# Kernel tuning notes

Measured on AMD Instinct MI355X. Metric: run time of the kernel, lower is better.

The kernel has to match this reference:

```python
import jax, jax.numpy as jnp
import numpy as np
import math

B, S, H = 2, 2048, 1024
NH, HD = 16, 64
MAX_SCALE = 4


def setup_inputs() -> dict:
    key = jax.random.key(0)
    ks = jax.random.split(key, 8)
    s = 0.02
    return {
        "x": jax.random.normal(ks[0], (B, S, H), dtype=jnp.float32),
        "Wqkv": jax.random.normal(ks[1], (H, 3 * H), dtype=jnp.float32) * s,
        "bqkv": jnp.zeros((3 * H,), dtype=jnp.float32),
        "Wout": jax.random.normal(ks[2], (H, H), dtype=jnp.float32) * s,
        "bout": jnp.zeros((H,), dtype=jnp.float32),
        "Wscale": jax.random.normal(ks[3], (H, MAX_SCALE), dtype=jnp.float32) * s,
        "bscale": jnp.zeros((MAX_SCALE,), dtype=jnp.float32),
    }


def reference(x, Wqkv, bqkv, Wout, bout, Wscale, bscale):
    b, s, h = x.shape
    inv_sqrt_hd = 1.0 / math.sqrt(HD)
    # qkv projection -> [3, b, nh, s, hd]
    qkv = (x @ Wqkv + bqkv).reshape(b, s, 3, NH, HD).transpose(2, 0, 3, 1, 4)
    q, k, v = qkv[0], qkv[1], qkv[2]
    # per-token soft weights over scales [b, s, max_scale]
    scale_weights = jax.nn.softmax(x @ Wscale + bscale, axis=-1)
    out = jnp.zeros((b, NH, s, HD), dtype=x.dtype)
    for scale_idx in range(MAX_SCALE):
        dilation = 2 ** scale_idx
        kd = k[:, :, ::dilation]  # strided (dilated) gather of keys
        vd = v[:, :, ::dilation]
        scores = jnp.einsum("bhqd,bhkd->bhqk", q, kd) * inv_sqrt_hd
        attn = jax.nn.softmax(scores, axis=-1)
        o = jnp.einsum("bhqk,bhkd->bhqd", attn, vd)
        w = scale_weights[:, :, scale_idx][:, None, :, None]  # [b,1,s,1]
        out = out + o * w
    out = out.transpose(0, 2, 1, 3).reshape(b, s, h)
    return out @ Wout + bout
```

## Files before the change

kernel.cpp:

```cpp
#include <hip/hip_runtime.h>
#include <stdint.h>

typedef unsigned short u16;
typedef __attribute__((ext_vector_type(8))) __bf16 bf8v;
typedef __attribute__((ext_vector_type(4))) float f4v;
typedef __attribute__((ext_vector_type(16))) float f16v;

#define BB 2
#define SS 2048
#define HH 1024

#define OFF_Q   0u
#define OFF_K0  8388608u
#define OFF_K1  16777216u
#define OFF_K2  20971520u
#define OFF_K3  23068672u
#define OFF_V0  24117248u
#define OFF_V1  32505856u
#define OFF_V2  36700160u
#define OFF_V3  38797312u
#define OFF_WQT 39845888u
#define OFF_WOT 46137344u
#define OFF_SCW 48234496u

__device__ __forceinline__ u16 f2bf(float f) {
    union { float f; uint32_t u; } v; v.f = f;
    uint32_t r = v.u + 0x7fffu + ((v.u >> 16) & 1u);
    return (u16)(r >> 16);
}
__device__ __forceinline__ uint32_t pk2(float a, float b) {
    return (uint32_t)f2bf(a) | ((uint32_t)f2bf(b) << 16);
}

__global__ __launch_bounds__(256) void wconv_kernel(const float* __restrict__ W,
                                                    u16* __restrict__ Wt,
                                                    int N, int K) {
    __shared__ float tile[64][69];
    const int tid = threadIdx.x;
    const int n0 = blockIdx.x * 64, k0 = blockIdx.y * 64;
    const int r = tid >> 4, c4 = (tid & 15) * 4;
#pragma unroll
    for (int it = 0; it < 4; it++) {
        float4 v = *(const float4*)&W[(size_t)(k0 + it * 16 + r) * N + n0 + c4];
        tile[it * 16 + r][c4 + 0] = v.x; tile[it * 16 + r][c4 + 1] = v.y;
        tile[it * 16 + r][c4 + 2] = v.z; tile[it * 16 + r][c4 + 3] = v.w;
    }
    __syncthreads();
#pragma unroll
    for (int it = 0; it < 4; it++) {
        int n = it * 16 + r;
        uint2 pk;
        pk.x = pk2(tile[c4 + 0][n], tile[c4 + 1][n]);
        pk.y = pk2(tile[c4 + 2][n], tile[c4 + 3][n]);
        *(uint2*)&Wt[(size_t)(n0 + n) * K + k0 + c4] = pk;
    }
}

__global__ __launch_bounds__(256) void scale_kernel(const float* __restrict__ x,
                                                    const float* __restrict__ Wscale,
                                                    const float* __restrict__ bscale,
                                                    float* __restrict__ scw) {
    const int lane = threadIdx.x & 63;
    const int wid  = threadIdx.x >> 6;
    const int row  = blockIdx.x * 4 + wid;
    float a0 = 0.f, a1 = 0.f, a2 = 0.f, a3 = 0.f;
    for (int i = 0; i < 16; i++) {
        int hh = lane + i * 64;
        float xs = x[(size_t)row * HH + hh];
        float4 wv = *(const float4*)&Wscale[hh * 4];
        a0 += xs * wv.x; a1 += xs * wv.y; a2 += xs * wv.z; a3 += xs * wv.w;
    }
    for (int off = 1; off < 64; off <<= 1) {
        a0 += __shfl_xor(a0, off); a1 += __shfl_xor(a1, off);
        a2 += __shfl_xor(a2, off); a3 += __shfl_xor(a3, off);
    }
    if (lane == 0) {
        a0 += bscale[0]; a1 += bscale[1]; a2 += bscale[2]; a3 += bscale[3];
        float mx = fmaxf(fmaxf(a0, a1), fmaxf(a2, a3));
        float e0 = __expf(a0 - mx), e1 = __expf(a1 - mx);
        float e2 = __expf(a2 - mx), e3 = __expf(a3 - mx);
        float inv = 1.f / (e0 + e1 + e2 + e3);
        float4 o = {e0 * inv, e1 * inv, e2 * inv, e3 * inv};
        *(float4*)&scw[(size_t)row * 4] = o;
    }
}

template<int MODE, bool ABF16>
__global__ __launch_bounds__(256) void gemm_bt(const void* __restrict__ Ap,
                                               const u16* __restrict__ Bt,
                                               const float* __restrict__ bias,
                                               void* __restrict__ Cp,
                                               int N, int K) {
    __shared__ __align__(16) u16 At[128 * 40];
    __shared__ __align__(16) u16 Btl[128 * 40];
    const int tid  = threadIdx.x;
    const int lane = tid & 63;
    const int wid  = tid >> 6;
    const int l15  = lane & 15;
    const int quad = lane >> 4;
    const int wm = wid & 1, wn = wid >> 1;
    const int m0 = blockIdx.y * 128;
    const int n0 = blockIdx.x * 128;
    const int srow = tid >> 2;
    const int sc8  = (tid & 3) * 8;

    f4v acc[4][4];
#pragma unroll
    for (int i = 0; i < 4; i++)
#pragma unroll
        for (int j = 0; j < 4; j++) acc[i][j] = (f4v){0.f, 0.f, 0.f, 0.f};

    uint4 pa0, pa1;
    float4 fa00, fa01, fa10, fa11;
    if (ABF16) {
        const u16* Ab = (const u16*)Ap;
        pa0 = *(const uint4*)(Ab + (size_t)(m0 + srow) * K + sc8);
        pa1 = *(const uint4*)(Ab + (size_t)(m0 + srow + 64) * K + sc8);
    } else {
        const float* Af = (const float*)Ap;
        fa00 = *(const float4*)(Af + (size_t)(m0 + srow) * K + sc8);
        fa01 = *(const float4*)(Af + (size_t)(m0 + srow) * K + sc8 + 4);
        fa10 = *(const float4*)(Af + (size_t)(m0 + srow + 64) * K + sc8);
        fa11 = *(const float4*)(Af + (size_t)(m0 + srow + 64) * K + sc8 + 4);
    }
    uint4 pb0 = *(const uint4*)(Bt + (size_t)(n0 + srow) * K + sc8);
    uint4 pb1 = *(const uint4*)(Bt + (size_t)(n0 + srow + 64) * K + sc8);

    for (int kc = 0; kc < K; kc += 32) {
        __syncthreads();
        if (ABF16) {
            *(uint4*)&At[srow * 40 + sc8]        = pa0;
            *(uint4*)&At[(srow + 64) * 40 + sc8] = pa1;
        } else {
            uint4 w0, w1;
            w0.x = pk2(fa00.x, fa00.y); w0.y = pk2(fa00.z, fa00.w);
            w0.z = pk2(fa01.x, fa01.y); w0.w = pk2(fa01.z, fa01.w);
            w1.x = pk2(fa10.x, fa10.y); w1.y = pk2(fa10.z, fa10.w);
            w1.z = pk2(fa11.x, fa11.y); w1.w = pk2(fa11.z, fa11.w);
            *(uint4*)&At[srow * 40 + sc8]        = w0;
            *(uint4*)&At[(srow + 64) * 40 + sc8] = w1;
        }
        *(uint4*)&Btl[srow * 40 + sc8]        = pb0;
        *(uint4*)&Btl[(srow + 64) * 40 + sc8] = pb1;
        __syncthreads();
        if (kc + 32 < K) {
            if (ABF16) {
                const u16* Ab = (const u16*)Ap;
                pa0 = *(const uint4*)(Ab + (size_t)(m0 + srow) * K + kc + 32 + sc8);
                pa1 = *(const uint4*)(Ab + (size_t)(m0 + srow + 64) * K + kc + 32 + sc8);
            } else {
                const float* Af = (const float*)Ap;
                fa00 = *(const float4*)(Af + (size_t)(m0 + srow) * K + kc + 32 + sc8);
                fa01 = *(const float4*)(Af + (size_t)(m0 + srow) * K + kc + 32 + sc8 + 4);
                fa10 = *(const float4*)(Af + (size_t)(m0 + srow + 64) * K + kc + 32 + sc8);
                fa11 = *(const float4*)(Af + (size_t)(m0 + srow + 64) * K + kc + 32 + sc8 + 4);
            }
            pb0 = *(const uint4*)(Bt + (size_t)(n0 + srow) * K + kc + 32 + sc8);
            pb1 = *(const uint4*)(Bt + (size_t)(n0 + srow + 64) * K + kc + 32 + sc8);
        }
        bf8v af[4], bf[4];
#pragma unroll
        for (int t = 0; t < 4; t++) {
            af[t] = *(const bf8v*)&At[(wm * 64 + t * 16 + l15) * 40 + quad * 8];
            bf[t] = *(const bf8v*)&Btl[(wn * 64 + t * 16 + l15) * 40 + quad * 8];
        }
#pragma unroll
        for (int ti = 0; ti < 4; ti++)
#pragma unroll
            for (int tj = 0; tj < 4; tj++)
                acc[ti][tj] = __builtin_amdgcn_mfma_f32_16x16x32_bf16(af[ti], bf[tj], acc[ti][tj], 0, 0, 0);
    }

    if (MODE == 0) {
#pragma unroll
        for (int ti = 0; ti < 4; ti++)
#pragma unroll
            for (int tj = 0; tj < 4; tj++)
#pragma unroll
                for (int r = 0; r < 4; r++) {
                    int m = m0 + wm * 64 + ti * 16 + quad * 4 + r;
                    int n = n0 + wn * 64 + tj * 16 + l15;
                    ((float*)Cp)[(size_t)m * N + n] = acc[ti][tj][r] + bias[n];
                }
    } else {
        char* ws = (char*)Cp;
        u16* Qd = (u16*)ws;
        u16* K0 = (u16*)(ws + OFF_K0); u16* K1 = (u16*)(ws + OFF_K1);
        u16* K2 = (u16*)(ws + OFF_K2); u16* K3 = (u16*)(ws + OFF_K3);
        u16* V0 = (u16*)(ws + OFF_V0); u16* V1 = (u16*)(ws + OFF_V1);
        u16* V2 = (u16*)(ws + OFF_V2); u16* V3 = (u16*)(ws + OFF_V3);
        const int region = n0 >> 10;
        if (region == 0) {
#pragma unroll
            for (int ti = 0; ti < 4; ti++)
#pragma unroll
                for (int tj = 0; tj < 4; tj++)
#pragma unroll
                    for (int r = 0; r < 4; r++) {
                        int m = m0 + wm * 64 + ti * 16 + quad * 4 + r;
                        int n = n0 + wn * 64 + tj * 16 + l15;
                        Qd[(size_t)m * 1024 + n] = f2bf(acc[ti][tj][r] + bias[n]);
                    }
        } else if (region == 1) {
#pragma unroll
            for (int ti = 0; ti < 4; ti++)
#pragma unroll
                for (int tj = 0; tj < 4; tj++) {
                    int n  = n0 + wn * 64 + tj * 16 + l15;
                    int nk = n - 1024;
                    int h = nk >> 6, hd = nk & 63;
#pragma unroll
                    for (int r = 0; r < 4; r++) {
                        int m = m0 + wm * 64 + ti * 16 + quad * 4 + r;
                        int bb = m >> 11, tok = m & 2047;
                        int bh = bb * 16 + h;
                        u16 bv = f2bf((acc[ti][tj][r] + bias[n]) * 0.125f);
                        K0[((size_t)bh * 2048 + tok) * 64 + hd] = bv;
                        if (!(r & 1)) K1[((size_t)bh * 1024 + (tok >> 1)) * 64 + hd] = bv;
                        if (r == 0) {
                            K2[((size_t)bh * 512 + (tok >> 2)) * 64 + hd] = bv;
                            if (!(quad & 1)) K3[((size_t)bh * 256 + (tok >> 3)) * 64 + hd] = bv;
                        }
                    }
                }
        } else {
#pragma unroll
            for (int ti = 0; ti < 4; ti++)
#pragma unroll
                for (int tj = 0; tj < 4; tj++) {
                    int n  = n0 + wn * 64 + tj * 16 + l15;
                    int nv = n - 2048;
                    int h = nv >> 6, hd = nv & 63;
                    int tokb = m0 + wm * 64 + ti * 16 + quad * 4;
                    int bb = tokb >> 11, tok = tokb & 2047;
                    int bh = bb * 16 + h;
                    float v0 = acc[ti][tj][0] + bias[n];
                    float v1 = acc[ti][tj][1] + bias[n];
                    float v2 = acc[ti][tj][2] + bias[n];
                    float v3 = acc[ti][tj][3] + bias[n];
                    u16 c0 = f2bf(v0), c1 = f2bf(v1), c2 = f2bf(v2), c3 = f2bf(v3);
                    uint2 pk;
                    pk.x = (uint32_t)c0 | ((uint32_t)c1 << 16);
                    pk.y = (uint32_t)c2 | ((uint32_t)c3 << 16);
                    *(uint2*)&V0[((size_t)bh * 64 + hd) * 2048 + tok] = pk;
                    *(uint32_t*)&V1[((size_t)bh * 64 + hd) * 1024 + (tok >> 1)] =
                        (uint32_t)c0 | ((uint32_t)c2 << 16);
                    V2[((size_t)bh * 64 + hd) * 512 + (tok >> 2)] = c0;
                    if (!(quad & 1)) V3[((size_t)bh * 64 + hd) * 256 + (tok >> 3)] = c0;
                }
        }
    }
}

__global__ __launch_bounds__(128, 1) void attn_kernel(const char* __restrict__ ws) {
    __shared__ __align__(16) u16 Kt[32 * 72];
    __shared__ __align__(16) u16 Vt[64 * 40];
    __shared__ __align__(16) u16 Pt[2 * 64 * 40];

    const u16* Qd    = (const u16*)(ws + OFF_Q);
    const float* scw = (const float*)(ws + OFF_SCW);
    u16* attnb       = (u16*)(ws + OFF_Q);

    const int tid  = threadIdx.x;
    const int lane = tid & 63;
    const int wid  = tid >> 6;
    const int l31  = lane & 31;
    const int half = lane >> 5;
    const int b = blockIdx.z, h = blockIdx.y;
    const int qb = blockIdx.x * 128 + wid * 64;
    const int bh = b * 16 + h;

    const int skey = tid >> 3;
    const int shd8 = (tid & 7) * 8;
    const int svhd = tid >> 2;
    const int svk8 = (tid & 3) * 8;

    bf8v qf[2][4];
#pragma unroll
    for (int qt = 0; qt < 2; qt++)
#pragma unroll
        for (int ks = 0; ks < 4; ks++)
            qf[qt][ks] = *(const bf8v*)(Qd + (size_t)(b * SS + qb + qt * 32 + l31) * 1024
                                        + h * 64 + ks * 16 + half * 8);

    u16* Pw = Pt + wid * (64 * 40);

    f16v ofin[2][2];
#pragma unroll
    for (int qt = 0; qt < 2; qt++)
#pragma unroll
        for (int ht = 0; ht < 2; ht++)
#pragma unroll
            for (int r = 0; r < 16; r++) ofin[qt][ht][r] = 0.f;

    const uint32_t koff[4] = {OFF_K0, OFF_K1, OFF_K2, OFF_K3};
    const uint32_t voff[4] = {OFF_V0, OFF_V1, OFF_V2, OFF_V3};

#pragma unroll
    for (int s = 0; s < 4; s++) {
        const int Ss = SS >> s;
        const int nch = Ss >> 5;
        const u16* Kb = (const u16*)(ws + koff[s]) + (size_t)bh * Ss * 64;
        const u16* Vb = (const u16*)(ws + voff[s]) + (size_t)bh * 64 * Ss;

        f16v oacc[2][2];
#pragma unroll
        for (int qt = 0; qt < 2; qt++)
#pragma unroll
            for (int ht = 0; ht < 2; ht++)
#pragma unroll
                for (int r = 0; r < 16; r++) oacc[qt][ht][r] = 0.f;
        float ls0 = 0.f, ls1 = 0.f;

        uint4 kr0 = *(const uint4*)(Kb + (size_t)skey * 64 + shd8);
        uint4 kr1 = *(const uint4*)(Kb + (size_t)(skey + 16) * 64 + shd8);
        uint4 vr0 = *(const uint4*)(Vb + (size_t)svhd * Ss + svk8);
        uint4 vr1 = *(const uint4*)(Vb + (size_t)(svhd + 32) * Ss + svk8);

        for (int c = 0; c < nch; c++) {
            __syncthreads();
            *(uint4*)&Kt[skey * 72 + shd8]        = kr0;
            *(uint4*)&Kt[(skey + 16) * 72 + shd8] = kr1;
            *(uint4*)&Vt[svhd * 40 + svk8]        = vr0;
            *(uint4*)&Vt[(svhd + 32) * 40 + svk8] = vr1;
            __syncthreads();
            if (c + 1 < nch) {
                kr0 = *(const uint4*)(Kb + (size_t)((c + 1) * 32 + skey) * 64 + shd8);
                kr1 = *(const uint4*)(Kb + (size_t)((c + 1) * 32 + skey + 16) * 64 + shd8);
                vr0 = *(const uint4*)(Vb + (size_t)svhd * Ss + (c + 1) * 32 + svk8);
                vr1 = *(const uint4*)(Vb + (size_t)(svhd + 32) * Ss + (c + 1) * 32 + svk8);
            }
            f16v sa0, sa1;
#pragma unroll
            for (int r = 0; r < 16; r++) { sa0[r] = 0.f; sa1[r] = 0.f; }
#pragma unroll
            for (int ks = 0; ks < 4; ks++) {
                bf8v ka = *(const bf8v*)&Kt[l31 * 72 + ks * 16 + half * 8];
                sa0 = __builtin_amdgcn_mfma_f32_32x32x16_bf16(ka, qf[0][ks], sa0, 0, 0, 0);
                sa1 = __builtin_amdgcn_mfma_f32_32x32x16_bf16(ka, qf[1][ks], sa1, 0, 0, 0);
            }
#pragma unroll
            for (int qt = 0; qt < 2; qt++) {
                const f16v& sa = qt ? sa1 : sa0;
                float e[16];
#pragma unroll
                for (int r = 0; r < 16; r++) e[r] = __expf(sa[r]);
                float acc = 0.f;
#pragma unroll
                for (int r = 0; r < 16; r++) acc += e[r];
                if (qt) ls1 += acc; else ls0 += acc;
#pragma unroll
                for (int g = 0; g < 4; g++) {
                    uint2 pk;
                    pk.x = pk2(e[g * 4 + 0], e[g * 4 + 1]);
                    pk.y = pk2(e[g * 4 + 2], e[g * 4 + 3]);
                    *(uint2*)&Pw[(qt * 32 + l31) * 40 + g * 8 + half * 4] = pk;
                }
            }
            __asm__ volatile("s_waitcnt lgkmcnt(0)" ::: "memory");
#pragma unroll
            for (int kst = 0; kst < 2; kst++) {
                bf8v pb0 = *(const bf8v*)&Pw[l31 * 40 + kst * 16 + half * 8];
                bf8v pb1 = *(const bf8v*)&Pw[(32 + l31) * 40 + kst * 16 + half * 8];
#pragma unroll
                for (int ht = 0; ht < 2; ht++) {
                    bf8v va = *(const bf8v*)&Vt[(ht * 32 + l31) * 40 + kst * 16 + half * 8];
                    oacc[0][ht] = __builtin_amdgcn_mfma_f32_32x32x16_bf16(va, pb0, oacc[0][ht], 0, 0, 0);
                    oacc[1][ht] = __builtin_amdgcn_mfma_f32_32x32x16_bf16(va, pb1, oacc[1][ht], 0, 0, 0);
                }
            }
        }
#pragma unroll
        for (int qt = 0; qt < 2; qt++) {
            float l = qt ? ls1 : ls0;
            l += __shfl_xor(l, 32);
            float w = scw[(size_t)(b * SS + qb + qt * 32 + l31) * 4 + s] / l;
#pragma unroll
            for (int ht = 0; ht < 2; ht++)
#pragma unroll
                for (int r = 0; r < 16; r++) ofin[qt][ht][r] += w * oacc[qt][ht][r];
        }
    }
#pragma unroll
    for (int qt = 0; qt < 2; qt++) {
        const size_t base = (size_t)(b * SS + qb + qt * 32 + l31) * 1024 + h * 64;
#pragma unroll
        for (int ht = 0; ht < 2; ht++)
#pragma unroll
            for (int g = 0; g < 4; g++) {
                uint2 pk;
                pk.x = pk2(ofin[qt][ht][g * 4 + 0], ofin[qt][ht][g * 4 + 1]);
                pk.y = pk2(ofin[qt][ht][g * 4 + 2], ofin[qt][ht][g * 4 + 3]);
                *(uint2*)&attnb[base + ht * 32 + g * 8 + half * 4] = pk;
            }
    }
}

extern "C" void kernel_launch(void* const* d_in, const int* in_sizes, int n_in,
                              void* d_out, int out_size, void* d_ws, size_t ws_size,
                              hipStream_t stream) {
    const float* x      = (const float*)d_in[0];
    const float* Wqkv   = (const float*)d_in[1];
    const float* bqkv   = (const float*)d_in[2];
    const float* Wout   = (const float*)d_in[3];
    const float* bout   = (const float*)d_in[4];
    const float* Wscale = (const float*)d_in[5];
    const float* bscale = (const float*)d_in[6];
    float* out = (float*)d_out;

    char* ws = (char*)d_ws;
    u16*   wqt   = (u16*)(ws + OFF_WQT);
    u16*   wot   = (u16*)(ws + OFF_WOT);
    u16*   attnb = (u16*)(ws + OFF_Q);
    float* scw   = (float*)(ws + OFF_SCW);

    wconv_kernel<<<dim3(48, 16), dim3(256), 0, stream>>>(Wqkv, wqt, 3072, 1024);
    wconv_kernel<<<dim3(16, 16), dim3(256), 0, stream>>>(Wout, wot, 1024, 1024);
    scale_kernel<<<dim3(1024), dim3(256), 0, stream>>>(x, Wscale, bscale, scw);
    gemm_bt<1, false><<<dim3(24, 32), dim3(256), 0, stream>>>(
        (const void*)x, wqt, bqkv, (void*)ws, 3072, 1024);
    attn_kernel<<<dim3(16, 16, 2), dim3(128), 0, stream>>>(ws);
    gemm_bt<0, true><<<dim3(8, 32), dim3(256), 0, stream>>>(
        (const void*)attnb, wot, bout, (void*)out, 1024, 1024);
}
```

Measured before the change: 314.2 us.

## Split attention scales across waves, per-wave LDS, pre-convert x to bf16

The attention kernel now gives each block 64 queries and splits the scales between its two waves. Wave 0 handles the full-length scale 0 and wave 1 handles the dilated scales 1 to 3, so the two waves do roughly equal work. Each wave gets its own LDS region for K, V and P, which removes the block-wide syncthreads inside the chunk loop. The two partial outputs are combined through LDS at the end, the grid is doubled, and launch bounds allow two blocks per CU. Separately, x is converted to bf16 in its own kernel so the QKV GEMM loads bf16 directly, and P is packed by truncation rather than round-to-nearest, which costs a little accuracy.

Result: slower. 445.2 us (+41.7%).

```diff
diff --git a/kernel.cpp b/kernel.cpp
--- a/kernel.cpp
+++ b/kernel.cpp
@@ -21,7 +21,8 @@
 #define OFF_V3  38797312u
 #define OFF_WQT 39845888u
 #define OFF_WOT 46137344u
-#define OFF_SCW 48234496u
+#define OFF_XB  48234496u
+#define OFF_SCW 56623104u
 
 __device__ __forceinline__ u16 f2bf(float f) {
     union { float f; uint32_t u; } v; v.f = f;
@@ -30,6 +31,18 @@
 }
 __device__ __forceinline__ uint32_t pk2(float a, float b) {
     return (uint32_t)f2bf(a) | ((uint32_t)f2bf(b) << 16);
+}
+__device__ __forceinline__ uint32_t pkt2(float a, float b) {
+    union { float f; uint32_t u; } x, y; x.f = a; y.f = b;
+    return (x.u >> 16) | (y.u & 0xffff0000u);
+}
+
+__global__ __launch_bounds__(256) void xconv_kernel(const float* __restrict__ x,
+                                                    u16* __restrict__ xb) {
+    size_t t = (size_t)blockIdx.x * 256 + threadIdx.x;
+    float4 v = *(const float4*)&x[t * 4];
+    uint2 pk; pk.x = pk2(v.x, v.y); pk.y = pk2(v.z, v.w);
+    *(uint2*)&xb[t * 4] = pk;
 }
 
 __global__ __launch_bounds__(256) void wconv_kernel(const float* __restrict__ W,
@@ -85,8 +98,8 @@
     }
 }
 
-template<int MODE, bool ABF16>
-__global__ __launch_bounds__(256) void gemm_bt(const void* __restrict__ Ap,
+template<int MODE>
+__global__ __launch_bounds__(256) void gemm_bt(const u16* __restrict__ A,
                                                const u16* __restrict__ Bt,
                                                const float* __restrict__ bias,
                                                void* __restrict__ Cp,
@@ -110,51 +123,21 @@
 #pragma unroll
         for (int j = 0; j < 4; j++) acc[i][j] = (f4v){0.f, 0.f, 0.f, 0.f};
 
-    uint4 pa0, pa1;
-    float4 fa00, fa01, fa10, fa11;
-    if (ABF16) {
-        const u16* Ab = (const u16*)Ap;
-        pa0 = *(const uint4*)(Ab + (size_t)(m0 + srow) * K + sc8);
-        pa1 = *(const uint4*)(Ab + (size_t)(m0 + srow + 64) * K + sc8);
-    } else {
-        const float* Af = (const float*)Ap;
-        fa00 = *(const float4*)(Af + (size_t)(m0 + srow) * K + sc8);
-        fa01 = *(const float4*)(Af + (size_t)(m0 + srow) * K + sc8 + 4);
-        fa10 = *(const float4*)(Af + (size_t)(m0 + srow + 64) * K + sc8);
-        fa11 = *(const float4*)(Af + (size_t)(m0 + srow + 64) * K + sc8 + 4);
-    }
+    uint4 pa0 = *(const uint4*)(A  + (size_t)(m0 + srow) * K + sc8);
+    uint4 pa1 = *(const uint4*)(A  + (size_t)(m0 + srow + 64) * K + sc8);
     uint4 pb0 = *(const uint4*)(Bt + (size_t)(n0 + srow) * K + sc8);
     uint4 pb1 = *(const uint4*)(Bt + (size_t)(n0 + srow + 64) * K + sc8);
 
     for (int kc = 0; kc < K; kc += 32) {
         __syncthreads();
-        if (ABF16) {
-            *(uint4*)&At[srow * 40 + sc8]        = pa0;
-            *(uint4*)&At[(srow + 64) * 40 + sc8] = pa1;
-        } else {
-            uint4 w0, w1;
-            w0.x = pk2(fa00.x, fa00.y); w0.y = pk2(fa00.z, fa00.w);
-            w0.z = pk2(fa01.x, fa01.y); w0.w = pk2(fa01.z, fa01.w);
-            w1.x = pk2(fa10.x, fa10.y); w1.y = pk2(fa10.z, fa10.w);
-            w1.z = pk2(fa11.x, fa11.y); w1.w = pk2(fa11.z, fa11.w);
-            *(uint4*)&At[srow * 40 + sc8]        = w0;
-            *(uint4*)&At[(srow + 64) * 40 + sc8] = w1;
-        }
+        *(uint4*)&At[srow * 40 + sc8]         = pa0;
+        *(uint4*)&At[(srow + 64) * 40 + sc8]  = pa1;
         *(uint4*)&Btl[srow * 40 + sc8]        = pb0;
         *(uint4*)&Btl[(srow + 64) * 40 + sc8] = pb1;
         __syncthreads();
         if (kc + 32 < K) {
-            if (ABF16) {
-                const u16* Ab = (const u16*)Ap;
-                pa0 = *(const uint4*)(Ab + (size_t)(m0 + srow) * K + kc + 32 + sc8);
-                pa1 = *(const uint4*)(Ab + (size_t)(m0 + srow + 64) * K + kc + 32 + sc8);
-            } else {
-                const float* Af = (const float*)Ap;
-                fa00 = *(const float4*)(Af + (size_t)(m0 + srow) * K + kc + 32 + sc8);
-                fa01 = *(const float4*)(Af + (size_t)(m0 + srow) * K + kc + 32 + sc8 + 4);
-                fa10 = *(const float4*)(Af + (size_t)(m0 + srow + 64) * K + kc + 32 + sc8);
-                fa11 = *(const float4*)(Af + (size_t)(m0 + srow + 64) * K + kc + 32 + sc8 + 4);
-            }
+            pa0 = *(const uint4*)(A  + (size_t)(m0 + srow) * K + kc + 32 + sc8);
+            pa1 = *(const uint4*)(A  + (size_t)(m0 + srow + 64) * K + kc + 32 + sc8);
             pb0 = *(const uint4*)(Bt + (size_t)(n0 + srow) * K + kc + 32 + sc8);
             pb1 = *(const uint4*)(Bt + (size_t)(n0 + srow + 64) * K + kc + 32 + sc8);
         }
@@ -252,10 +235,9 @@
     }
 }
 
-__global__ __launch_bounds__(128, 1) void attn_kernel(const char* __restrict__ ws) {
-    __shared__ __align__(16) u16 Kt[32 * 72];
-    __shared__ __align__(16) u16 Vt[64 * 40];
-    __shared__ __align__(16) u16 Pt[2 * 64 * 40];
+#define WLDS 14848
+__global__ __launch_bounds__(128, 2) void attn_kernel(const char* __restrict__ ws) {
+    __shared__ __align__(16) char smem[2 * WLDS];
 
     const u16* Qd    = (const u16*)(ws + OFF_Q);
     const float* scw = (const float*)(ws + OFF_SCW);
@@ -267,13 +249,21 @@
     const int l31  = lane & 31;
     const int half = lane >> 5;
     const int b = blockIdx.z, h = blockIdx.y;
-    const int qb = blockIdx.x * 128 + wid * 64;
+    const int qb = blockIdx.x * 64;
     const int bh = b * 16 + h;
 
-    const int skey = tid >> 3;
-    const int shd8 = (tid & 7) * 8;
-    const int svhd = tid >> 2;
-    const int svk8 = (tid & 3) * 8;
+    u16* Kt = (u16*)(smem + wid * WLDS);
+    u16* Vt = (u16*)(smem + wid * WLDS + 9216);
+    u16* Pw = (u16*)(smem + wid * WLDS + 9216 + 5120 ? 0 : 0, smem + wid * WLDS + 4608);
+    Kt = (u16*)(smem + wid * WLDS);
+    u16* Vt2 = (u16*)(smem + wid * WLDS + 4608);
+    u16* Pw2 = (u16*)(smem + wid * WLDS + 9728);
+    float* comb = (float*)smem;
+
+    const int skey = lane >> 3;
+    const int sgr  = lane & 7;
+    const int svr  = lane >> 2;
+    const int skg  = lane & 3;
 
     bf8v qf[2][4];
 #pragma unroll
@@ -283,8 +273,6 @@
             qf[qt][ks] = *(const bf8v*)(Qd + (size_t)(b * SS + qb + qt * 32 + l31) * 1024
                                         + h * 64 + ks * 16 + half * 8);
 
-    u16* Pw = Pt + wid * (64 * 40);
-
     f16v ofin[2][2];
 #pragma unroll
     for (int qt = 0; qt < 2; qt++)
@@ -295,9 +283,10 @@
 
     const uint32_t koff[4] = {OFF_K0, OFF_K1, OFF_K2, OFF_K3};
     const uint32_t voff[4] = {OFF_V0, OFF_V1, OFF_V2, OFF_V3};
-
-#pragma unroll
-    for (int s = 0; s < 4; s++) {
+    const int s_lo = wid ? 1 : 0;
+    const int s_hi = wid ? 3 : 0;
+
+    for (int s = s_lo; s <= s_hi; s++) {
         const int Ss = SS >> s;
         const int nch = Ss >> 5;
         const u16* Kb = (const u16*)(ws + koff[s]) + (size_t)bh * Ss * 64;
@@ -312,24 +301,25 @@
                 for (int r = 0; r < 16; r++) oacc[qt][ht][r] = 0.f;
         float ls0 = 0.f, ls1 = 0.f;
 
-        uint4 kr0 = *(const uint4*)(Kb + (size_t)skey * 64 + shd8);
-        uint4 kr1 = *(const uint4*)(Kb + (size_t)(skey + 16) * 64 + shd8);
-        uint4 vr0 = *(const uint4*)(Vb + (size_t)svhd * Ss + svk8);
-        uint4 vr1 = *(const uint4*)(Vb + (size_t)(svhd + 32) * Ss + svk8);
+        uint4 kr[4];
+#pragma unroll
+        for (int i = 0; i < 4; i++)
+            kr[i] = *(const uint4*)(Kb + (size_t)(i * 8 + skey) * 64 + sgr * 8);
 
         for (int c = 0; c < nch; c++) {
-            __syncthreads();
-            *(uint4*)&Kt[skey * 72 + shd8]        = kr0;
-            *(uint4*)&Kt[(skey + 16) * 72 + shd8] = kr1;
-            *(uint4*)&Vt[svhd * 40 + svk8]        = vr0;
-            *(uint4*)&Vt[(svhd + 32) * 40 + svk8] = vr1;
-            __syncthreads();
+            uint4 vr[4];
+#pragma unroll
+            for (int i = 0; i < 4; i++)
+                vr[i] = *(const uint4*)(Vb + (size_t)(i * 16 + svr) * Ss + c * 32 + skg * 8);
+#pragma unroll
+            for (int i = 0; i < 4; i++)
+                *(uint4*)&Kt[(i * 8 + skey) * 72 + sgr * 8] = kr[i];
             if (c + 1 < nch) {
-                kr0 = *(const uint4*)(Kb + (size_t)((c + 1) * 32 + skey) * 64 + shd8);
-                kr1 = *(const uint4*)(Kb + (size_t)((c + 1) * 32 + skey + 16) * 64 + shd8);
-                vr0 = *(const uint4*)(Vb + (size_t)svhd * Ss + (c + 1) * 32 + svk8);
-                vr1 = *(const uint4*)(Vb + (size_t)(svhd + 32) * Ss + (c + 1) * 32 + svk8);
+#pragma unroll
+                for (int i = 0; i < 4; i++)
+                    kr[i] = *(const uint4*)(Kb + (size_t)((c + 1) * 32 + i * 8 + skey) * 64 + sgr * 8);
             }
+            __asm__ volatile("s_waitcnt lgkmcnt(0)" ::: "memory");
             f16v sa0, sa1;
 #pragma unroll
             for (int r = 0; r < 16; r++) { sa0[r] = 0.f; sa1[r] = 0.f; }
@@ -342,29 +332,32 @@
 #pragma unroll
             for (int qt = 0; qt < 2; qt++) {
                 const f16v& sa = qt ? sa1 : sa0;
-                float e[16];
-#pragma unroll
-                for (int r = 0; r < 16; r++) e[r] = __expf(sa[r]);
-                float acc = 0.f;
-#pragma unroll
-                for (int r = 0; r < 16; r++) acc += e[r];
-                if (qt) ls1 += acc; else ls0 += acc;
+                float lq = 0.f;
 #pragma unroll
                 for (int g = 0; g < 4; g++) {
+                    float e0 = __expf(sa[g * 4 + 0]);
+                    float e1 = __expf(sa[g * 4 + 1]);
+                    float e2 = __expf(sa[g * 4 + 2]);
+                    float e3 = __expf(sa[g * 4 + 3]);
+                    lq += (e0 + e1) + (e2 + e3);
                     uint2 pk;
-                    pk.x = pk2(e[g * 4 + 0], e[g * 4 + 1]);
-                    pk.y = pk2(e[g * 4 + 2], e[g * 4 + 3]);
-                    *(uint2*)&Pw[(qt * 32 + l31) * 40 + g * 8 + half * 4] = pk;
-                }
+                    pk.x = pkt2(e0, e1);
+                    pk.y = pkt2(e2, e3);
+                    *(uint2*)&Pw2[(qt * 32 + l31) * 40 + g * 8 + half * 4] = pk;
+                }
+                if (qt) ls1 += lq; else ls0 += lq;
             }
+#pragma unroll
+            for (int i = 0; i < 4; i++)
+                *(uint4*)&Vt2[(i * 16 + svr) * 40 + skg * 8] = vr[i];
             __asm__ volatile("s_waitcnt lgkmcnt(0)" ::: "memory");
 #pragma unroll
             for (int kst = 0; kst < 2; kst++) {
-                bf8v pb0 = *(const bf8v*)&Pw[l31 * 40 + kst * 16 + half * 8];
-                bf8v pb1 = *(const bf8v*)&Pw[(32 + l31) * 40 + kst * 16 + half * 8];
+                bf8v pb0 = *(const bf8v*)&Pw2[l31 * 40 + kst * 16 + half * 8];
+                bf8v pb1 = *(const bf8v*)&Pw2[(32 + l31) * 40 + kst * 16 + half * 8];
 #pragma unroll
                 for (int ht = 0; ht < 2; ht++) {
-                    bf8v va = *(const bf8v*)&Vt[(ht * 32 + l31) * 40 + kst * 16 + half * 8];
+                    bf8v va = *(const bf8v*)&Vt2[(ht * 32 + l31) * 40 + kst * 16 + half * 8];
                     oacc[0][ht] = __builtin_amdgcn_mfma_f32_32x32x16_bf16(va, pb0, oacc[0][ht], 0, 0, 0);
                     oacc[1][ht] = __builtin_amdgcn_mfma_f32_32x32x16_bf16(va, pb1, oacc[1][ht], 0, 0, 0);
                 }
@@ -381,18 +374,42 @@
                 for (int r = 0; r < 16; r++) ofin[qt][ht][r] += w * oacc[qt][ht][r];
         }
     }
-#pragma unroll
-    for (int qt = 0; qt < 2; qt++) {
-        const size_t base = (size_t)(b * SS + qb + qt * 32 + l31) * 1024 + h * 64;
-#pragma unroll
-        for (int ht = 0; ht < 2; ht++)
-#pragma unroll
-            for (int g = 0; g < 4; g++) {
-                uint2 pk;
-                pk.x = pk2(ofin[qt][ht][g * 4 + 0], ofin[qt][ht][g * 4 + 1]);
-                pk.y = pk2(ofin[qt][ht][g * 4 + 2], ofin[qt][ht][g * 4 + 3]);
-                *(uint2*)&attnb[base + ht * 32 + g * 8 + half * 4] = pk;
-            }
+
+    __syncthreads();
+    if (wid == 1) {
+#pragma unroll
+        for (int qt = 0; qt < 2; qt++)
+#pragma unroll
+            for (int ht = 0; ht < 2; ht++)
+#pragma unroll
+                for (int g = 0; g < 4; g++) {
+                    int slot = qt * 8 + ht * 4 + g;
+                    float4 v = {ofin[qt][ht][g * 4 + 0], ofin[qt][ht][g * 4 + 1],
+                                ofin[qt][ht][g * 4 + 2], ofin[qt][ht][g * 4 + 3]};
+                    *(float4*)&comb[slot * 256 + lane * 4] = v;
+                }
+    }
+    __syncthreads();
+    if (wid == 0) {
+#pragma unroll
+        for (int qt = 0; qt < 2; qt++) {
+            const size_t base = (size_t)(b * SS + qb + qt * 32 + l31) * 1024 + h * 64;
+#pragma unroll
+            for (int ht = 0; ht < 2; ht++)
+#pragma unroll
+                for (int g = 0; g < 4; g++) {
+                    int slot = qt * 8 + ht * 4 + g;
+                    float4 v = *(const float4*)&comb[slot * 256 + lane * 4];
+                    float o0 = ofin[qt][ht][g * 4 + 0] + v.x;
+                    float o1 = ofin[qt][ht][g * 4 + 1] + v.y;
+                    float o2 = ofin[qt][ht][g * 4 + 2] + v.z;
+                    float o3 = ofin[qt][ht][g * 4 + 3] + v.w;
+                    uint2 pk;
+                    pk.x = pk2(o0, o1);
+                    pk.y = pk2(o2, o3);
+                    *(uint2*)&attnb[base + ht * 32 + g * 8 + half * 4] = pk;
+                }
+        }
     }
 }
 
@@ -411,15 +428,15 @@
     char* ws = (char*)d_ws;
     u16*   wqt   = (u16*)(ws + OFF_WQT);
     u16*   wot   = (u16*)(ws + OFF_WOT);
+    u16*   xb    = (u16*)(ws + OFF_XB);
     u16*   attnb = (u16*)(ws + OFF_Q);
     float* scw   = (float*)(ws + OFF_SCW);
 
+    xconv_kernel<<<dim3(4096), dim3(256), 0, stream>>>(x, xb);
     wconv_kernel<<<dim3(48, 16), dim3(256), 0, stream>>>(Wqkv, wqt, 3072, 1024);
     wconv_kernel<<<dim3(16, 16), dim3(256), 0, stream>>>(Wout, wot, 1024, 1024);
     scale_kernel<<<dim3(1024), dim3(256), 0, stream>>>(x, Wscale, bscale, scw);
-    gemm_bt<1, false><<<dim3(24, 32), dim3(256), 0, stream>>>(
-        (const void*)x, wqt, bqkv, (void*)ws, 3072, 1024);
-    attn_kernel<<<dim3(16, 16, 2), dim3(128), 0, stream>>>(ws);
-    gemm_bt<0, true><<<dim3(8, 32), dim3(256), 0, stream>>>(
-        (const void*)attnb, wot, bout, (void*)out, 1024, 1024);
-}
+    gemm_bt<1><<<dim3(24, 32), dim3(256), 0, stream>>>(xb, wqt, bqkv, (void*)ws, 3072, 1024);
+    attn_kernel<<<dim3(32, 16, 2), dim3(128), 0, stream>>>(ws);
+    gemm_bt<0><<<dim3(8, 32), dim3(256), 0, stream>>>(attnb, wot, bout, (void*)out, 1024, 1024);
+}
```
